# Kernel optimization log

Measured on AMD Instinct MI355X. Metric: run time of the kernel, lower is better.

Reference implementation:

```python
import jax, jax.numpy as jnp
import numpy as np

NUM_HEADS = 8

B, N, M = 2, 10000, 320000
QD = KD = HD = 256


def setup_inputs() -> dict:
    key = jax.random.key(0)
    k1, k2, k3, k4, k5 = jax.random.split(key, 5)
    x_q = jax.random.normal(k1, (B, N, QD), dtype=jnp.float32)
    x_k = jax.random.normal(k2, (B, N, KD), dtype=jnp.float32)
    mask = jax.random.randint(k3, (2, M), 0, N, dtype=jnp.int64)
    # xavier_uniform: limit = sqrt(6/(fan_in+fan_out))
    lim_q = float(np.sqrt(6.0 / (QD + HD)))
    lim_k = float(np.sqrt(6.0 / (KD + HD)))
    w_q = jax.random.uniform(k4, (QD, HD), minval=-lim_q, maxval=lim_q, dtype=jnp.float32)
    w_k = jax.random.uniform(k5, (KD, HD), minval=-lim_k, maxval=lim_k, dtype=jnp.float32)
    return {"x_q": x_q, "x_k": x_k, "mask": mask, "w_q": w_q, "w_k": w_k}


def reference(x_q, x_k, mask, w_q, w_k):
    b, n, _ = x_q.shape
    m = mask.shape[1]
    d = w_q.shape[1]          # hidden_dim
    h = NUM_HEADS
    dh = d // h
    q = x_q @ w_q             # (b, n, d)
    k = x_k @ w_k             # (b, n, d)
    # edge gather + elementwise multiply
    prod = q[:, mask[0], :] * k[:, mask[1], :]            # (b, m, d)
    # head buffer is i // (d/h): contiguous blocks -> reshape-sum
    a = prod.reshape(b, m, h, dh).sum(axis=-1)            # (b, m, h)
    a = a / jnp.sqrt(jnp.float32(w_k.shape[0]))           # / sqrt(key_dim)
    # segment softmax over destination index = mask[1 - reduce_dim], reduce_dim=1 -> mask[0]
    idx = mask[0]
    a = a - a.max()                                       # global max, as in source
    e = jnp.exp(a)                                        # (b, m, h)
    seg = jnp.zeros((b, n, h), e.dtype).at[:, idx, :].add(e)
    return e / (seg[:, idx, :] + 1e-16)
```

## Files before the change

kernel.cpp:

```cpp
#include <hip/hip_runtime.h>
#include <hip/hip_bf16.h>
#include <hip/hip_fp16.h>

#define DHID 256
#define NHEAD 8
#define BATCH 2

typedef _Float16 h8 __attribute__((ext_vector_type(8)));
typedef float f4 __attribute__((ext_vector_type(4)));

__global__ __launch_bounds__(256) void prep_kernel(
    const float* __restrict__ Wq, const float* __restrict__ Wk,
    _Float16* __restrict__ Wtq, _Float16* __restrict__ Wtk,
    float* __restrict__ seg, int segN)
{
    if (blockIdx.z == 2) {
        int idx = (blockIdx.x * 8 + blockIdx.y) * 256 + threadIdx.y * 32 + threadIdx.x;
        for (int i = idx; i < segN; i += 64 * 256) seg[i] = 0.f;
        return;
    }
    const float* W = blockIdx.z ? Wk : Wq;
    _Float16* Wt   = blockIdx.z ? Wtk : Wtq;
    __shared__ float tile[32][33];
    const int tx = threadIdx.x;
    const int ty = threadIdx.y;
    const int n0 = blockIdx.x * 32;
    const int k0 = blockIdx.y * 32;
#pragma unroll
    for (int j = 0; j < 32; j += 8)
        tile[ty + j][tx] = W[(size_t)(k0 + ty + j) * DHID + n0 + tx];
    __syncthreads();
#pragma unroll
    for (int j = 0; j < 32; j += 8)
        Wt[(size_t)(n0 + ty + j) * DHID + k0 + tx] = (_Float16)tile[tx][ty + j];
}

__global__ __launch_bounds__(256, 2) void gemm_mfma(
    const float* __restrict__ Xq, const float* __restrict__ Xk,
    const _Float16* __restrict__ Wtq, const _Float16* __restrict__ Wtk,
    _Float16* __restrict__ Qh, _Float16* __restrict__ Kh, int Mrows)
{
    const float* X       = blockIdx.z ? Xk : Xq;
    const _Float16* Wt   = blockIdx.z ? Wtk : Wtq;
    _Float16* C          = blockIdx.z ? Kh : Qh;

    __shared__ _Float16 As[64 * 256];
    __shared__ _Float16 Bs[64 * 256];

    const int t    = threadIdx.x;
    const int lane = t & 63;
    const int wave = t >> 6;
    const int rowBase = blockIdx.x * 64;

#pragma unroll
    for (int i = 0; i < 8; ++i) {
        int idx = t + i * 256;
        int row = idx >> 5;
        int c   = idx & 31;
        int grow = rowBase + row;
        f4 v0 = {0,0,0,0}, v1 = {0,0,0,0};
        if (grow < Mrows) {
            const float* p = X + (size_t)grow * DHID + c * 8;
            v0 = *(const f4*)p;
            v1 = *(const f4*)(p + 4);
        }
        h8 hv;
        hv[0]=(_Float16)v0[0]; hv[1]=(_Float16)v0[1]; hv[2]=(_Float16)v0[2]; hv[3]=(_Float16)v0[3];
        hv[4]=(_Float16)v1[0]; hv[5]=(_Float16)v1[1]; hv[6]=(_Float16)v1[2]; hv[7]=(_Float16)v1[3];
        int sc = c ^ (row & 7);
        *(h8*)&As[row * 256 + sc * 8] = hv;
    }

    const int ar   = wave * 16 + (lane & 15);
    const int quad = lane >> 4;

    for (int ct64 = 0; ct64 < 4; ++ct64) {
#pragma unroll
        for (int i = 0; i < 8; ++i) {
            int idx = t + i * 256;
            int n = idx >> 5;
            int c = idx & 31;
            h8 hv = *(const h8*)(Wt + (size_t)(ct64 * 64 + n) * DHID + c * 8);
            int sc = c ^ (n & 7);
            *(h8*)&Bs[n * 256 + sc * 8] = hv;
        }
        __syncthreads();

        f4 acc[4] = {{0,0,0,0},{0,0,0,0},{0,0,0,0},{0,0,0,0}};
#pragma unroll
        for (int kc = 0; kc < 8; ++kc) {
            int ac = (kc * 4 + quad) ^ (ar & 7);
            h8 afrag = *(const h8*)&As[ar * 256 + ac * 8];
#pragma unroll
            for (int ct = 0; ct < 4; ++ct) {
                int bn = ct * 16 + (lane & 15);
                int bc = (kc * 4 + quad) ^ (bn & 7);
                h8 bfrag = *(const h8*)&Bs[bn * 256 + bc * 8];
                acc[ct] = __builtin_amdgcn_mfma_f32_16x16x32_f16(afrag, bfrag, acc[ct], 0, 0, 0);
            }
        }

#pragma unroll
        for (int ct = 0; ct < 4; ++ct) {
#pragma unroll
            for (int r = 0; r < 4; ++r) {
                int grow = rowBase + wave * 16 + quad * 4 + r;
                if (grow < Mrows)
                    C[(size_t)grow * DHID + ct64 * 64 + ct * 16 + (lane & 15)] = (_Float16)acc[ct][r];
            }
        }
        __syncthreads();
    }
}

__global__ __launch_bounds__(256, 6) void edge_kernel(
    const _Float16* __restrict__ Qh, const _Float16* __restrict__ Kh,
    const int* __restrict__ mask, float* __restrict__ out,
    float* __restrict__ seg, int M, int N)
{
    const int lane = threadIdx.x & 63;
    const int wave = threadIdx.x >> 6;
    const int c    = lane & 31;
    const int half = lane >> 5;
    const int h    = c >> 2;
    const long e0 = ((long)blockIdx.x * 4 + wave) * 8;
    const int b = blockIdx.y;
    if (e0 >= M) return;

    int idxv = 0;
    {
        long le = e0 + (lane & 7);
        if (le >= M) le = M - 1;
        if (lane < 8)       idxv = mask[le];
        else if (lane < 16) idxv = mask[M + le];
    }

    const _Float16* Qb = Qh + (size_t)b * N * DHID;
    const _Float16* Kb = Kh + (size_t)b * N * DHID;

    int sidx[4], didx[4];
#pragma unroll
    for (int p = 0; p < 4; ++p) {
        sidx[p] = __shfl(idxv, p * 2 + half);
        didx[p] = __shfl(idxv, 8 + p * 2 + half);
    }

    h8 qv[4], kv[4];
#pragma unroll
    for (int p = 0; p < 4; ++p) {
        qv[p] = *(const h8*)(Qb + (size_t)sidx[p] * DHID + c * 8);
        kv[p] = *(const h8*)(Kb + (size_t)didx[p] * DHID + c * 8);
    }

#pragma unroll
    for (int p = 0; p < 4; ++p) {
        float s = 0.f;
#pragma unroll
        for (int u = 0; u < 8; ++u)
            s += (float)qv[p][u] * (float)kv[p][u];
        s += __shfl_xor(s, 1);
        s += __shfl_xor(s, 2);
        float ev = expf(s * 0.0625f);
        const long e = e0 + p * 2 + half;
        if ((c & 3) == 0 && e < M) {
            __builtin_nontemporal_store(ev, &out[((size_t)b * M + e) * NHEAD + h]);
            atomicAdd(seg + ((size_t)b * N + sidx[p]) * NHEAD + h, ev);
        }
    }
}

__global__ __launch_bounds__(256) void norm_kernel(
    const int* __restrict__ mask, const float* __restrict__ seg,
    float* __restrict__ out, int M, int N, int BM)
{
    int idx = blockIdx.x * 256 + threadIdx.x;
    if (idx >= BM) return;
    int b = idx / M;
    int e = idx - b * M;
    int src = mask[e];
    const f4* s4 = (const f4*)(seg + ((size_t)b * N + src) * NHEAD);
    f4 s0 = s4[0], s1 = s4[1];
    f4* o4 = (f4*)(out + (size_t)idx * NHEAD);
    f4 o0 = o4[0], o1 = o4[1];
    o0[0] *= __builtin_amdgcn_rcpf(s0[0] + 1e-16f);
    o0[1] *= __builtin_amdgcn_rcpf(s0[1] + 1e-16f);
    o0[2] *= __builtin_amdgcn_rcpf(s0[2] + 1e-16f);
    o0[3] *= __builtin_amdgcn_rcpf(s0[3] + 1e-16f);
    o1[0] *= __builtin_amdgcn_rcpf(s1[0] + 1e-16f);
    o1[1] *= __builtin_amdgcn_rcpf(s1[1] + 1e-16f);
    o1[2] *= __builtin_amdgcn_rcpf(s1[2] + 1e-16f);
    o1[3] *= __builtin_amdgcn_rcpf(s1[3] + 1e-16f);
    __builtin_nontemporal_store(o0, &o4[0]);
    __builtin_nontemporal_store(o1, &o4[1]);
}

extern "C" void kernel_launch(void* const* d_in, const int* in_sizes, int n_in,
                              void* d_out, int out_size, void* d_ws, size_t ws_size,
                              hipStream_t stream) {
    const float* x_q  = (const float*)d_in[0];
    const float* x_k  = (const float*)d_in[1];
    const int*   mask = (const int*)d_in[2];
    const float* w_q  = (const float*)d_in[3];
    const float* w_k  = (const float*)d_in[4];
    float* out = (float*)d_out;

    const int M = in_sizes[2] / 2;
    const int N = in_sizes[0] / (BATCH * DHID);
    const int Mrows = BATCH * N;

    _Float16* Qh  = (_Float16*)d_ws;
    _Float16* Kh  = Qh  + (size_t)Mrows * DHID;
    _Float16* Wtq = Kh  + (size_t)Mrows * DHID;
    _Float16* Wtk = Wtq + (size_t)DHID * DHID;
    float*    seg = (float*)(Wtk + (size_t)DHID * DHID);

    prep_kernel<<<dim3(DHID / 32, DHID / 32, 3), dim3(32, 8), 0, stream>>>(
        w_q, w_k, Wtq, Wtk, seg, BATCH * N * NHEAD);

    dim3 ggrid((Mrows + 63) / 64, 1, 2);
    gemm_mfma<<<ggrid, 256, 0, stream>>>(x_q, x_k, Wtq, Wtk, Qh, Kh, Mrows);

    long waves = (M + 7) / 8;
    dim3 egrid((unsigned)((waves + 3) / 4), BATCH);
    edge_kernel<<<egrid, 256, 0, stream>>>(Qh, Kh, mask, out, seg, M, N);

    const int BM = BATCH * M;
    norm_kernel<<<(BM + 255) / 256, 256, 0, stream>>>(mask, seg, out, M, N, BM);
}
```

Before: 181.6 us.

## Store unnormalized exps as fp16 intermediate and merge Q/K GEMMs per block

The edge kernel now writes exp scores as fp16 into a workspace buffer instead of fp32 into the output. The norm kernel reads them back and writes the fp32 normalized result, so it no longer does a read-modify-write of the fp32 output. This cuts intermediate traffic on the memory-bound edge/norm path but lowers precision of the stored exps. Separately, the GEMM grid drops its z dimension and each block loops over both Q and K, halving block count.

```diff
diff --git a/kernel.cpp b/kernel.cpp
--- a/kernel.cpp
+++ b/kernel.cpp
@@ -40,10 +40,6 @@
     const _Float16* __restrict__ Wtq, const _Float16* __restrict__ Wtk,
     _Float16* __restrict__ Qh, _Float16* __restrict__ Kh, int Mrows)
 {
-    const float* X       = blockIdx.z ? Xk : Xq;
-    const _Float16* Wt   = blockIdx.z ? Wtk : Wtq;
-    _Float16* C          = blockIdx.z ? Kh : Qh;
-
     __shared__ _Float16 As[64 * 256];
     __shared__ _Float16 Bs[64 * 256];
 
@@ -51,71 +47,76 @@
     const int lane = t & 63;
     const int wave = t >> 6;
     const int rowBase = blockIdx.x * 64;
-
-#pragma unroll
-    for (int i = 0; i < 8; ++i) {
-        int idx = t + i * 256;
-        int row = idx >> 5;
-        int c   = idx & 31;
-        int grow = rowBase + row;
-        f4 v0 = {0,0,0,0}, v1 = {0,0,0,0};
-        if (grow < Mrows) {
-            const float* p = X + (size_t)grow * DHID + c * 8;
-            v0 = *(const f4*)p;
-            v1 = *(const f4*)(p + 4);
-        }
-        h8 hv;
-        hv[0]=(_Float16)v0[0]; hv[1]=(_Float16)v0[1]; hv[2]=(_Float16)v0[2]; hv[3]=(_Float16)v0[3];
-        hv[4]=(_Float16)v1[0]; hv[5]=(_Float16)v1[1]; hv[6]=(_Float16)v1[2]; hv[7]=(_Float16)v1[3];
-        int sc = c ^ (row & 7);
-        *(h8*)&As[row * 256 + sc * 8] = hv;
-    }
-
     const int ar   = wave * 16 + (lane & 15);
     const int quad = lane >> 4;
 
-    for (int ct64 = 0; ct64 < 4; ++ct64) {
+    for (int z = 0; z < 2; ++z) {
+        const float* X     = z ? Xk : Xq;
+        const _Float16* Wt = z ? Wtk : Wtq;
+        _Float16* C        = z ? Kh : Qh;
+
 #pragma unroll
         for (int i = 0; i < 8; ++i) {
             int idx = t + i * 256;
-            int n = idx >> 5;
-            int c = idx & 31;
-            h8 hv = *(const h8*)(Wt + (size_t)(ct64 * 64 + n) * DHID + c * 8);
-            int sc = c ^ (n & 7);
-            *(h8*)&Bs[n * 256 + sc * 8] = hv;
+            int row = idx >> 5;
+            int c   = idx & 31;
+            int grow = rowBase + row;
+            f4 v0 = {0,0,0,0}, v1 = {0,0,0,0};
+            if (grow < Mrows) {
+                const float* p = X + (size_t)grow * DHID + c * 8;
+                v0 = *(const f4*)p;
+                v1 = *(const f4*)(p + 4);
+            }
+            h8 hv;
+            hv[0]=(_Float16)v0[0]; hv[1]=(_Float16)v0[1]; hv[2]=(_Float16)v0[2]; hv[3]=(_Float16)v0[3];
+            hv[4]=(_Float16)v1[0]; hv[5]=(_Float16)v1[1]; hv[6]=(_Float16)v1[2]; hv[7]=(_Float16)v1[3];
+            int sc = c ^ (row & 7);
+            *(h8*)&As[row * 256 + sc * 8] = hv;
         }
-        __syncthreads();
-
-        f4 acc[4] = {{0,0,0,0},{0,0,0,0},{0,0,0,0},{0,0,0,0}};
-#pragma unroll
-        for (int kc = 0; kc < 8; ++kc) {
-            int ac = (kc * 4 + quad) ^ (ar & 7);
-            h8 afrag = *(const h8*)&As[ar * 256 + ac * 8];
+
+        for (int ct64 = 0; ct64 < 4; ++ct64) {
+#pragma unroll
+            for (int i = 0; i < 8; ++i) {
+                int idx = t + i * 256;
+                int n = idx >> 5;
+                int c = idx & 31;
+                h8 hv = *(const h8*)(Wt + (size_t)(ct64 * 64 + n) * DHID + c * 8);
+                int sc = c ^ (n & 7);
+                *(h8*)&Bs[n * 256 + sc * 8] = hv;
+            }
+            __syncthreads();
+
+            f4 acc[4] = {{0,0,0,0},{0,0,0,0},{0,0,0,0},{0,0,0,0}};
+#pragma unroll
+            for (int kc = 0; kc < 8; ++kc) {
+                int ac = (kc * 4 + quad) ^ (ar & 7);
+                h8 afrag = *(const h8*)&As[ar * 256 + ac * 8];
+#pragma unroll
+                for (int ct = 0; ct < 4; ++ct) {
+                    int bn = ct * 16 + (lane & 15);
+                    int bc = (kc * 4 + quad) ^ (bn & 7);
+                    h8 bfrag = *(const h8*)&Bs[bn * 256 + bc * 8];
+                    acc[ct] = __builtin_amdgcn_mfma_f32_16x16x32_f16(afrag, bfrag, acc[ct], 0, 0, 0);
+                }
+            }
+
 #pragma unroll
             for (int ct = 0; ct < 4; ++ct) {
-                int bn = ct * 16 + (lane & 15);
-                int bc = (kc * 4 + quad) ^ (bn & 7);
-                h8 bfrag = *(const h8*)&Bs[bn * 256 + bc * 8];
-                acc[ct] = __builtin_amdgcn_mfma_f32_16x16x32_f16(afrag, bfrag, acc[ct], 0, 0, 0);
-            }
+#pragma unroll
+                for (int r = 0; r < 4; ++r) {
+                    int grow = rowBase + wave * 16 + quad * 4 + r;
+                    if (grow < Mrows)
+                        C[(size_t)grow * DHID + ct64 * 64 + ct * 16 + (lane & 15)] = (_Float16)acc[ct][r];
+                }
+            }
+            __syncthreads();
         }
-
-#pragma unroll
-        for (int ct = 0; ct < 4; ++ct) {
-#pragma unroll
-            for (int r = 0; r < 4; ++r) {
-                int grow = rowBase + wave * 16 + quad * 4 + r;
-                if (grow < Mrows)
-                    C[(size_t)grow * DHID + ct64 * 64 + ct * 16 + (lane & 15)] = (_Float16)acc[ct][r];
-            }
-        }
-        __syncthreads();
     }
 }
 
 __global__ __launch_bounds__(256, 6) void edge_kernel(
     const _Float16* __restrict__ Qh, const _Float16* __restrict__ Kh,
-    const int* __restrict__ mask, float* __restrict__ out,
+    const int* __restrict__ mask, _Float16* __restrict__ eh,
     float* __restrict__ seg, int M, int N)
 {
     const int lane = threadIdx.x & 63;
@@ -160,18 +161,19 @@
             s += (float)qv[p][u] * (float)kv[p][u];
         s += __shfl_xor(s, 1);
         s += __shfl_xor(s, 2);
-        float ev = expf(s * 0.0625f);
         const long e = e0 + p * 2 + half;
         if ((c & 3) == 0 && e < M) {
-            __builtin_nontemporal_store(ev, &out[((size_t)b * M + e) * NHEAD + h]);
-            atomicAdd(seg + ((size_t)b * N + sidx[p]) * NHEAD + h, ev);
+            _Float16 evh = (_Float16)expf(s * 0.0625f);
+            __builtin_nontemporal_store(evh, &eh[((size_t)b * M + e) * NHEAD + h]);
+            atomicAdd(seg + ((size_t)b * N + sidx[p]) * NHEAD + h, (float)evh);
         }
     }
 }
 
 __global__ __launch_bounds__(256) void norm_kernel(
     const int* __restrict__ mask, const float* __restrict__ seg,
-    float* __restrict__ out, int M, int N, int BM)
+    const _Float16* __restrict__ eh, float* __restrict__ out,
+    int M, int N, int BM)
 {
     int idx = blockIdx.x * 256 + threadIdx.x;
     if (idx >= BM) return;
@@ -180,16 +182,17 @@
     int src = mask[e];
     const f4* s4 = (const f4*)(seg + ((size_t)b * N + src) * NHEAD);
     f4 s0 = s4[0], s1 = s4[1];
+    h8 ev = *(const h8*)(eh + (size_t)idx * NHEAD);
+    f4 o0, o1;
+    o0[0] = (float)ev[0] * __builtin_amdgcn_rcpf(s0[0] + 1e-16f);
+    o0[1] = (float)ev[1] * __builtin_amdgcn_rcpf(s0[1] + 1e-16f);
+    o0[2] = (float)ev[2] * __builtin_amdgcn_rcpf(s0[2] + 1e-16f);
+    o0[3] = (float)ev[3] * __builtin_amdgcn_rcpf(s0[3] + 1e-16f);
+    o1[0] = (float)ev[4] * __builtin_amdgcn_rcpf(s1[0] + 1e-16f);
+    o1[1] = (float)ev[5] * __builtin_amdgcn_rcpf(s1[1] + 1e-16f);
+    o1[2] = (float)ev[6] * __builtin_amdgcn_rcpf(s1[2] + 1e-16f);
+    o1[3] = (float)ev[7] * __builtin_amdgcn_rcpf(s1[3] + 1e-16f);
     f4* o4 = (f4*)(out + (size_t)idx * NHEAD);
-    f4 o0 = o4[0], o1 = o4[1];
-    o0[0] *= __builtin_amdgcn_rcpf(s0[0] + 1e-16f);
-    o0[1] *= __builtin_amdgcn_rcpf(s0[1] + 1e-16f);
-    o0[2] *= __builtin_amdgcn_rcpf(s0[2] + 1e-16f);
-    o0[3] *= __builtin_amdgcn_rcpf(s0[3] + 1e-16f);
-    o1[0] *= __builtin_amdgcn_rcpf(s1[0] + 1e-16f);
-    o1[1] *= __builtin_amdgcn_rcpf(s1[1] + 1e-16f);
-    o1[2] *= __builtin_amdgcn_rcpf(s1[2] + 1e-16f);
-    o1[3] *= __builtin_amdgcn_rcpf(s1[3] + 1e-16f);
     __builtin_nontemporal_store(o0, &o4[0]);
     __builtin_nontemporal_store(o1, &o4[1]);
 }
@@ -213,17 +216,18 @@
     _Float16* Wtq = Kh  + (size_t)Mrows * DHID;
     _Float16* Wtk = Wtq + (size_t)DHID * DHID;
     float*    seg = (float*)(Wtk + (size_t)DHID * DHID);
+    _Float16* eh  = (_Float16*)(seg + (size_t)BATCH * N * NHEAD);
 
     prep_kernel<<<dim3(DHID / 32, DHID / 32, 3), dim3(32, 8), 0, stream>>>(
         w_q, w_k, Wtq, Wtk, seg, BATCH * N * NHEAD);
 
-    dim3 ggrid((Mrows + 63) / 64, 1, 2);
-    gemm_mfma<<<ggrid, 256, 0, stream>>>(x_q, x_k, Wtq, Wtk, Qh, Kh, Mrows);
+    gemm_mfma<<<dim3((Mrows + 63) / 64), 256, 0, stream>>>(
+        x_q, x_k, Wtq, Wtk, Qh, Kh, Mrows);
 
     long waves = (M + 7) / 8;
     dim3 egrid((unsigned)((waves + 3) / 4), BATCH);
-    edge_kernel<<<egrid, 256, 0, stream>>>(Qh, Kh, mask, out, seg, M, N);
+    edge_kernel<<<egrid, 256, 0, stream>>>(Qh, Kh, mask, eh, seg, M, N);
 
     const int BM = BATCH * M;
-    norm_kernel<<<(BM + 255) / 256, 256, 0, stream>>>(mask, seg, out, M, N, BM);
-}
+    norm_kernel<<<(BM + 255) / 256, 256, 0, stream>>>(mask, seg, eh, out, M, N, BM);
+}
```

New measurement: 184.2 us. Within noise of the previous version (+1.4%).
